# Optimization experiments

Measured on AMD Instinct MI355X. Metric: run time of the kernel, lower is better.

Reference implementation:

```python
import jax, jax.numpy as jnp
import numpy as np

LMAX = 5
DIMS = [2 * l + 1 for l in range(LMAX + 1)]
S = sum(d * d for d in DIMS)  # 286 = sum_l (2l+1)^2 (mul_l = dim_l = 2l+1)
F_IN, F_OUT = 128, 128
B = 512
N_GRID = 512


def setup_inputs() -> dict:
    key = jax.random.key(0)
    k1, k2, k3 = jax.random.split(key, 3)
    # x: signal over SO(3) irreps, shape (B, f_in, S)
    x = jax.random.normal(k1, (B, F_IN, S), dtype=jnp.float32)
    # w: learned spatial filter, shape (f_in, f_out, n_grid) (nn.Parameter, normal init)
    w = jax.random.normal(k2, (F_IN, F_OUT, N_GRID), dtype=jnp.float32)
    # D: flattened Wigner-D buffer, shape (n_grid, S). Stand-in random values;
    # the forward math is identical to the true Wigner-D buffer.
    D = jax.random.normal(k3, (N_GRID, S), dtype=jnp.float32)
    return {"x": x, "w": w, "D": D}


def _so3_linear(x, psi):
    """e3nn o3.Linear over so3_irreps(LMAX) with external weights psi.

    Per degree l: x_l (B, f_in, 2l+1 [mul], 2l+1 [dim]),
    psi_l (f_in, f_out, mul_in, mul_out); mix multiplicities and f channels,
    with fan-in normalization 1/sqrt(f_in * mul_in).
    """
    bsz = x.shape[0]
    outs = []
    off = 0
    for l in range(LMAX + 1):
        d = 2 * l + 1
        blk = d * d
        x_l = x[:, :, off:off + blk].reshape(bsz, F_IN, d, d)
        w_l = psi[:, :, off:off + blk].reshape(F_IN, F_OUT, d, d)
        scale = 1.0 / np.sqrt(F_IN * d).astype(np.float32)
        y_l = jnp.einsum('bxui,xyuv->byvi', x_l, w_l) * scale
        outs.append(y_l.reshape(bsz, F_OUT, blk))
        off += blk
    return jnp.concatenate(outs, axis=-1)


def reference(x, w, D):
    # project spatial filter into harmonic (Fourier) domain
    psi = jnp.einsum('ni,xyn->xyi', D, w) / np.float32(np.sqrt(N_GRID))
    return _so3_linear(x, psi)
```

## Files before the change

kernel.cpp:

```cpp
#include <hip/hip_runtime.h>
#include <hip/hip_bf16.h>


#define NT 256
typedef __bf16 bf16x8 __attribute__((ext_vector_type(8)));
typedef float f32x4 __attribute__((ext_vector_type(4)));
typedef unsigned int u32;

__device__ __forceinline__ void gload_lds16(const void* g, void* l) {
  __builtin_amdgcn_global_load_lds(
      (const __attribute__((address_space(1))) u32*)g,
      (__attribute__((address_space(3))) u32*)l, 16, 0, 0);
}

__device__ __forceinline__ void decode_s(int s, int& off, int& d) {
  if (s >= 165)      { off = 165; d = 11; }
  else if (s >= 84)  { off = 84;  d = 9; }
  else if (s >= 35)  { off = 35;  d = 7; }
  else if (s >= 10)  { off = 10;  d = 5; }
  else if (s >= 1)   { off = 1;   d = 3; }
  else               { off = 0;   d = 1; }
}

template<int D, int OFF>
__device__ __forceinline__ void build_one(const float* __restrict__ X,
                                          __hip_bfloat16* __restrict__ A,
                                          int b, __hip_bfloat16* sm) {
  const float* src = X + (size_t)b * (128 * 286) + OFF;
  for (int e = threadIdx.x; e < 128 * D * D; e += NT) {
    const int x = e / (D * D), r = e - x * (D * D);
    sm[e] = __float2bfloat16(src[x * 286 + r]);
  }
  __syncthreads();
  __hip_bfloat16* dst = A + (size_t)65536 * OFF + (size_t)b * (D * 128 * D);
  for (int o = threadIdx.x; o < D * 128 * D; o += NT) {
    const int i = o / (128 * D);
    const int rem = o - i * (128 * D);
    const int x = rem / D, u = rem - x * D;
    dst[o] = sm[x * D * D + u * D + i];
  }
}

__global__ __launch_bounds__(NT)
void prep_all(const float* __restrict__ w, const float* __restrict__ Dm,
              const float* __restrict__ X,
              __hip_bfloat16* __restrict__ wb, __hip_bfloat16* __restrict__ DT,
              __hip_bfloat16* __restrict__ A) {
  __shared__ __hip_bfloat16 sm[128 * 121];
  const int bx = blockIdx.x;
  if (bx < 4096) {
    const int t = bx * NT + threadIdx.x;
    const float4 a = reinterpret_cast<const float4*>(w)[t * 2];
    const float4 b = reinterpret_cast<const float4*>(w)[t * 2 + 1];
    __hip_bfloat16 v[8];
    v[0] = __float2bfloat16(a.x); v[1] = __float2bfloat16(a.y);
    v[2] = __float2bfloat16(a.z); v[3] = __float2bfloat16(a.w);
    v[4] = __float2bfloat16(b.x); v[5] = __float2bfloat16(b.y);
    v[6] = __float2bfloat16(b.z); v[7] = __float2bfloat16(b.w);
    *reinterpret_cast<bf16x8*>(&wb[t * 8]) = *reinterpret_cast<bf16x8*>(v);
  } else if (bx < 4864) {
    const int e = (bx - 4096) * NT + threadIdx.x;
    const int s = e >> 9, g = e & 511;
    DT[e] = (s < 286) ? __float2bfloat16(Dm[g * 286 + s]) : __float2bfloat16(0.0f);
  } else {
    const int b2 = bx - 4864;
    if (b2 < 512)       build_one<11, 165>(X, A, b2, sm);
    else if (b2 < 1024) build_one<9, 84>(X, A, b2 - 512, sm);
    else if (b2 < 1536) build_one<7, 35>(X, A, b2 - 1024, sm);
    else if (b2 < 2048) build_one<5, 10>(X, A, b2 - 1536, sm);
    else if (b2 < 2560) build_one<3, 1>(X, A, b2 - 2048, sm);
    else                build_one<1, 0>(X, A, b2 - 2560, sm);
  }
}

__device__ __forceinline__ void stage_tile(
    const __hip_bfloat16* __restrict__ Ap, const __hip_bfloat16* __restrict__ Bp,
    int LDK, int ktv, int m0, int n0, int tid, int wave,
    __hip_bfloat16* sA, __hip_bfloat16* sB) {
#pragma unroll
  for (int c = 0; c < 4; ++c) {
    const int q = c * 256 + tid;
    const int row = q >> 3, slot = q & 7;
    const int scol = ((slot ^ (row & 7)) << 3);
    gload_lds16(&Ap[(m0 + row) * LDK + ktv + scol], &sA[(c * 256 + wave * 64) << 3]);
    gload_lds16(&Bp[(n0 + row) * LDK + ktv + scol], &sB[(c * 256 + wave * 64) << 3]);
  }
}

__device__ __forceinline__ void load_frags(
    const __hip_bfloat16* sA, const __hip_bfloat16* sB,
    int wr, int wc, int r15, int khi, bf16x8 (&af)[4][2], bf16x8 (&bf)[4][2]) {
#pragma unroll
  for (int m = 0; m < 4; ++m)
#pragma unroll
    for (int kk = 0; kk < 2; ++kk) {
      const int row = wr * 64 + m * 16 + r15;
      const int slot = (kk * 4 + khi) ^ (row & 7);
      af[m][kk] = *reinterpret_cast<const bf16x8*>(&sA[row * 64 + slot * 8]);
    }
#pragma unroll
  for (int n = 0; n < 4; ++n)
#pragma unroll
    for (int kk = 0; kk < 2; ++kk) {
      const int row = wc * 64 + n * 16 + r15;
      const int slot = (kk * 4 + khi) ^ (row & 7);
      bf[n][kk] = *reinterpret_cast<const bf16x8*>(&sB[row * 64 + slot * 8]);
    }
}

__device__ __forceinline__ void do_mfma(
    const bf16x8 (&af)[4][2], const bf16x8 (&bf)[4][2], f32x4 (&acc)[4][4]) {
#pragma unroll
  for (int kk = 0; kk < 2; ++kk)
#pragma unroll
    for (int m = 0; m < 4; ++m)
#pragma unroll
      for (int n = 0; n < 4; ++n)
        acc[m][n] = __builtin_amdgcn_mfma_f32_16x16x32_bf16(
            af[m][kk], bf[n][kk], acc[m][n], 0, 0, 0);
}

__global__ __launch_bounds__(NT)
void psi_mfma(const __hip_bfloat16* __restrict__ wb,
              const __hip_bfloat16* __restrict__ DT,
              __hip_bfloat16* __restrict__ PT) {
  const int m0 = blockIdx.x * 128, n0 = blockIdx.y * 128;

  __shared__ __hip_bfloat16 sA[2][128 * 64];
  __shared__ __hip_bfloat16 sB[2][128 * 64];

  const int tid = threadIdx.x;
  const int lane = tid & 63, wave = tid >> 6;
  const int wr = wave & 1, wc = wave >> 1;
  const int r15 = lane & 15, khi = lane >> 4;

  f32x4 acc[4][4] = {};
  bf16x8 af[4][2], bf[4][2];

  stage_tile(wb, DT, 512, 0, m0, n0, tid, wave, sA[0], sB[0]);
  __syncthreads();
  int cur = 0;
  for (int t = 0; t < 8; ++t) {
    if (t + 1 < 8)
      stage_tile(wb, DT, 512, (t + 1) << 6, m0, n0, tid, wave, sA[cur ^ 1], sB[cur ^ 1]);
    load_frags(sA[cur], sB[cur], wr, wc, r15, khi, af, bf);
    do_mfma(af, bf, acc);
    if (t + 1 < 8) { __syncthreads(); cur ^= 1; }
  }

#pragma unroll
  for (int n = 0; n < 4; ++n) {
    const int s = n0 + wc * 64 + n * 16 + r15;
    if (s >= 286) continue;
    int off, d;
    decode_s(s, off, d);
    const int rel = s - off;
    const int u = rel / d, v = rel - u * d;
    const float scale = 1.0f / (256.0f * sqrtf((float)d));
    __hip_bfloat16* Pl = PT + off * 16384;
    const int Kd = 128 * d;
#pragma unroll
    for (int m = 0; m < 4; ++m)
#pragma unroll
      for (int j = 0; j < 4; ++j) {
        const int row = m0 + wr * 64 + m * 16 + khi * 4 + j;
        const int x = row >> 7, y = row & 127;
        Pl[(y * d + v) * Kd + (x * d + u)] = __float2bfloat16(acc[m][n][j] * scale);
      }
  }
}

__global__ __launch_bounds__(NT)
void main_gemm(const __hip_bfloat16* __restrict__ Aall,
               const __hip_bfloat16* __restrict__ PTall,
               float* __restrict__ out) {
  int bx = blockIdx.x;
  int off, d;
  if (bx < 484)       { off = 165; d = 11; }
  else if (bx < 808)  { off = 84;  d = 9;  bx -= 484; }
  else if (bx < 1004) { off = 35;  d = 7;  bx -= 808; }
  else if (bx < 1104) { off = 10;  d = 5;  bx -= 1004; }
  else if (bx < 1140) { off = 1;   d = 3;  bx -= 1104; }
  else                { off = 0;   d = 1;  bx -= 1140; }
  const int bm = bx % (4 * d);
  const int bn = bx / (4 * d);
  const int Kn = 128 * d;
  const __hip_bfloat16* A  = Aall  + 65536 * off;
  const __hip_bfloat16* BT = PTall + 16384 * off;
  const int m0 = bm * 128, n0 = bn * 128;

  __shared__ __hip_bfloat16 sA[2][128 * 64];
  __shared__ __hip_bfloat16 sB[2][128 * 64];

  const int tid = threadIdx.x;
  const int lane = tid & 63, wave = tid >> 6;
  const int wr = wave & 1, wc = wave >> 1;
  const int r15 = lane & 15, khi = lane >> 4;

  f32x4 acc[4][4] = {};
  bf16x8 af[4][2], bf[4][2];

  const int nk = Kn >> 6;
  stage_tile(A, BT, Kn, 0, m0, n0, tid, wave, sA[0], sB[0]);
  __syncthreads();
  int cur = 0;
  for (int t = 0; t < nk; ++t) {
    if (t + 1 < nk)
      stage_tile(A, BT, Kn, (t + 1) << 6, m0, n0, tid, wave, sA[cur ^ 1], sB[cur ^ 1]);
    load_frags(sA[cur], sB[cur], wr, wc, r15, khi, af, bf);
    do_mfma(af, bf, acc);
    if (t + 1 < nk) { __syncthreads(); cur ^= 1; }
  }

  int yo4[4], v4[4];
#pragma unroll
  for (int n = 0; n < 4; ++n) {
    const int col = n0 + wc * 64 + n * 16 + r15;
    yo4[n] = col / d;
    v4[n] = col - yo4[n] * d;
  }
#pragma unroll
  for (int m = 0; m < 4; ++m)
#pragma unroll
    for (int j = 0; j < 4; ++j) {
      const int row = m0 + wr * 64 + m * 16 + khi * 4 + j;
      const int bb = row / d, i = row - bb * d;
      float* orow = out + (size_t)bb * 36608 + off + i;
#pragma unroll
      for (int n = 0; n < 4; ++n)
        orow[yo4[n] * 286 + v4[n] * d] = acc[m][n][j];
    }
}

extern "C" void kernel_launch(void* const* d_in, const int* in_sizes, int n_in,
                              void* d_out, int out_size, void* d_ws, size_t ws_size,
                              hipStream_t stream) {
  const float* x  = (const float*)d_in[0];
  const float* w  = (const float*)d_in[1];
  const float* Dm = (const float*)d_in[2];
  float* out = (float*)d_out;

  __hip_bfloat16* PT = (__hip_bfloat16*)d_ws;
  __hip_bfloat16* A  = PT + 16384 * 286;
  __hip_bfloat16* wb = A + 65536 * 286;
  __hip_bfloat16* DT = wb + 16384 * 512;

  prep_all<<<dim3(7936), dim3(NT), 0, stream>>>(w, Dm, x, wb, DT, A);
  psi_mfma<<<dim3(128, 3), dim3(NT), 0, stream>>>(wb, DT, PT);
  main_gemm<<<dim3(1144), dim3(NT), 0, stream>>>(A, PT, out);
}
```

Baseline: 161.8 us.

## Co-schedule x-layout build blocks with psi GEMM in one launch

```diff
diff --git a/kernel.cpp b/kernel.cpp
--- a/kernel.cpp
+++ b/kernel.cpp
@@ -22,31 +22,9 @@
   else               { off = 0;   d = 1; }
 }
 
-template<int D, int OFF>
-__device__ __forceinline__ void build_one(const float* __restrict__ X,
-                                          __hip_bfloat16* __restrict__ A,
-                                          int b, __hip_bfloat16* sm) {
-  const float* src = X + (size_t)b * (128 * 286) + OFF;
-  for (int e = threadIdx.x; e < 128 * D * D; e += NT) {
-    const int x = e / (D * D), r = e - x * (D * D);
-    sm[e] = __float2bfloat16(src[x * 286 + r]);
-  }
-  __syncthreads();
-  __hip_bfloat16* dst = A + (size_t)65536 * OFF + (size_t)b * (D * 128 * D);
-  for (int o = threadIdx.x; o < D * 128 * D; o += NT) {
-    const int i = o / (128 * D);
-    const int rem = o - i * (128 * D);
-    const int x = rem / D, u = rem - x * D;
-    dst[o] = sm[x * D * D + u * D + i];
-  }
-}
-
 __global__ __launch_bounds__(NT)
-void prep_all(const float* __restrict__ w, const float* __restrict__ Dm,
-              const float* __restrict__ X,
-              __hip_bfloat16* __restrict__ wb, __hip_bfloat16* __restrict__ DT,
-              __hip_bfloat16* __restrict__ A) {
-  __shared__ __hip_bfloat16 sm[128 * 121];
+void prep_wd(const float* __restrict__ w, const float* __restrict__ Dm,
+             __hip_bfloat16* __restrict__ wb, __hip_bfloat16* __restrict__ DT) {
   const int bx = blockIdx.x;
   if (bx < 4096) {
     const int t = bx * NT + threadIdx.x;
@@ -58,18 +36,10 @@
     v[4] = __float2bfloat16(b.x); v[5] = __float2bfloat16(b.y);
     v[6] = __float2bfloat16(b.z); v[7] = __float2bfloat16(b.w);
     *reinterpret_cast<bf16x8*>(&wb[t * 8]) = *reinterpret_cast<bf16x8*>(v);
-  } else if (bx < 4864) {
+  } else {
     const int e = (bx - 4096) * NT + threadIdx.x;
     const int s = e >> 9, g = e & 511;
     DT[e] = (s < 286) ? __float2bfloat16(Dm[g * 286 + s]) : __float2bfloat16(0.0f);
-  } else {
-    const int b2 = bx - 4864;
-    if (b2 < 512)       build_one<11, 165>(X, A, b2, sm);
-    else if (b2 < 1024) build_one<9, 84>(X, A, b2 - 512, sm);
-    else if (b2 < 1536) build_one<7, 35>(X, A, b2 - 1024, sm);
-    else if (b2 < 2048) build_one<5, 10>(X, A, b2 - 1536, sm);
-    else if (b2 < 2560) build_one<3, 1>(X, A, b2 - 2048, sm);
-    else                build_one<1, 0>(X, A, b2 - 2560, sm);
   }
 }
 
@@ -120,14 +90,31 @@
             af[m][kk], bf[n][kk], acc[m][n], 0, 0, 0);
 }
 
-__global__ __launch_bounds__(NT)
-void psi_mfma(const __hip_bfloat16* __restrict__ wb,
-              const __hip_bfloat16* __restrict__ DT,
-              __hip_bfloat16* __restrict__ PT) {
-  const int m0 = blockIdx.x * 128, n0 = blockIdx.y * 128;
-
-  __shared__ __hip_bfloat16 sA[2][128 * 64];
-  __shared__ __hip_bfloat16 sB[2][128 * 64];
+template<int D, int OFF>
+__device__ __forceinline__ void build_one(const float* __restrict__ X,
+                                          __hip_bfloat16* __restrict__ A,
+                                          int b, __hip_bfloat16* sm) {
+  const float* src = X + (size_t)b * (128 * 286) + OFF;
+  for (int e = threadIdx.x; e < 128 * D * D; e += NT) {
+    const int x = e / (D * D), r = e - x * (D * D);
+    sm[e] = __float2bfloat16(src[x * 286 + r]);
+  }
+  __syncthreads();
+  __hip_bfloat16* dst = A + (size_t)65536 * OFF + (size_t)b * (D * 128 * D);
+  for (int o = threadIdx.x; o < D * 128 * D; o += NT) {
+    const int i = o / (128 * D);
+    const int rem = o - i * (128 * D);
+    const int x = rem / D, u = rem - x * D;
+    dst[o] = sm[x * D * D + u * D + i];
+  }
+}
+
+__device__ __forceinline__ void psi_body(
+    const __hip_bfloat16* __restrict__ wb, const __hip_bfloat16* __restrict__ DT,
+    __hip_bfloat16* __restrict__ PT, int pb, __hip_bfloat16* smem) {
+  const int m0 = (pb & 127) * 128, n0 = (pb >> 7) * 128;
+  __hip_bfloat16* sAb[2] = { smem,         smem + 8192 };
+  __hip_bfloat16* sBb[2] = { smem + 16384, smem + 24576 };
 
   const int tid = threadIdx.x;
   const int lane = tid & 63, wave = tid >> 6;
@@ -137,13 +124,13 @@
   f32x4 acc[4][4] = {};
   bf16x8 af[4][2], bf[4][2];
 
-  stage_tile(wb, DT, 512, 0, m0, n0, tid, wave, sA[0], sB[0]);
+  stage_tile(wb, DT, 512, 0, m0, n0, tid, wave, sAb[0], sBb[0]);
   __syncthreads();
   int cur = 0;
   for (int t = 0; t < 8; ++t) {
     if (t + 1 < 8)
-      stage_tile(wb, DT, 512, (t + 1) << 6, m0, n0, tid, wave, sA[cur ^ 1], sB[cur ^ 1]);
-    load_frags(sA[cur], sB[cur], wr, wc, r15, khi, af, bf);
+      stage_tile(wb, DT, 512, (t + 1) << 6, m0, n0, tid, wave, sAb[cur ^ 1], sBb[cur ^ 1]);
+    load_frags(sAb[cur], sBb[cur], wr, wc, r15, khi, af, bf);
     do_mfma(af, bf, acc);
     if (t + 1 < 8) { __syncthreads(); cur ^= 1; }
   }
@@ -167,6 +154,28 @@
         const int x = row >> 7, y = row & 127;
         Pl[(y * d + v) * Kd + (x * d + u)] = __float2bfloat16(acc[m][n][j] * scale);
       }
+  }
+}
+
+__global__ __launch_bounds__(NT)
+void psi_build(const __hip_bfloat16* __restrict__ wb,
+               const __hip_bfloat16* __restrict__ DT,
+               __hip_bfloat16* __restrict__ PT,
+               const float* __restrict__ X,
+               __hip_bfloat16* __restrict__ A) {
+  __shared__ __align__(16) unsigned char smem[65536];
+  const int bx = blockIdx.x;
+  if (bx < 384) {
+    psi_body(wb, DT, PT, bx, (__hip_bfloat16*)smem);
+  } else {
+    __hip_bfloat16* sm = (__hip_bfloat16*)smem;
+    const int b2 = bx - 384;
+    if (b2 < 512)       build_one<11, 165>(X, A, b2, sm);
+    else if (b2 < 1024) build_one<9, 84>(X, A, b2 - 512, sm);
+    else if (b2 < 1536) build_one<7, 35>(X, A, b2 - 1024, sm);
+    else if (b2 < 2048) build_one<5, 10>(X, A, b2 - 1536, sm);
+    else if (b2 < 2560) build_one<3, 1>(X, A, b2 - 2048, sm);
+    else                build_one<1, 0>(X, A, b2 - 2560, sm);
   }
 }
 
@@ -245,7 +254,7 @@
   __hip_bfloat16* wb = A + 65536 * 286;
   __hip_bfloat16* DT = wb + 16384 * 512;
 
-  prep_all<<<dim3(7936), dim3(NT), 0, stream>>>(w, Dm, x, wb, DT, A);
-  psi_mfma<<<dim3(128, 3), dim3(NT), 0, stream>>>(wb, DT, PT);
+  prep_wd<<<dim3(4864), dim3(NT), 0, stream>>>(w, Dm, wb, DT);
+  psi_build<<<dim3(3456), dim3(NT), 0, stream>>>(wb, DT, PT, x, A);
   main_gemm<<<dim3(1144), dim3(NT), 0, stream>>>(A, PT, out);
 }
```

Measured after the change: 169.2 us. +4.5%, slower.
